# Kernel optimization log

Measured on AMD Instinct MI355X. Metric: run time of the kernel, lower is better.

## Reference

```python
import jax, jax.numpy as jnp
import numpy as np

N_NODES = 50000
N_EDGES = 800000
HIDDEN = 128
N_TYPES = 4
TIME_STEPS = [2]  # one layer, 2 propagation steps; residuals = {}


def setup_inputs() -> dict:
    key = jax.random.key(0)
    ks = jax.random.split(key, 8)
    std = HIDDEN ** (-0.5)
    states = jax.random.normal(ks[0], (N_NODES, HIDDEN), dtype=jnp.float32)
    etype = jax.random.randint(ks[1], (N_EDGES,), 0, N_TYPES, dtype=jnp.int32)
    src = jax.random.randint(ks[2], (N_EDGES,), 0, N_NODES, dtype=jnp.int32)
    tgt = jax.random.randint(ks[3], (N_EDGES,), 0, N_NODES, dtype=jnp.int32)
    edges = jnp.stack([etype, src, tgt], axis=1)  # [E, 3]: (type, source, target)
    type_weights = std * jax.random.normal(ks[4], (N_TYPES, HIDDEN, HIDDEN), dtype=jnp.float32)
    type_biases = std * jax.random.normal(ks[5], (N_TYPES, HIDDEN), dtype=jnp.float32)
    # Keras GRUCell (reset_after=True): kernel [H,3H], recurrent_kernel [H,3H], bias [2,3H]
    gru_kernel = std * jax.random.normal(ks[6], (HIDDEN, 3 * HIDDEN), dtype=jnp.float32)
    k7, k8 = jax.random.split(ks[7])
    gru_rec_kernel = std * jax.random.normal(k7, (HIDDEN, 3 * HIDDEN), dtype=jnp.float32)
    gru_bias = std * jax.random.normal(k8, (2, 3 * HIDDEN), dtype=jnp.float32)
    return {"states": states, "edges": edges, "type_weights": type_weights,
            "type_biases": type_biases, "gru_kernel": gru_kernel,
            "gru_rec_kernel": gru_rec_kernel, "gru_bias": gru_bias}


def _gru_cell(x, h, kernel, rec_kernel, bias):
    # Keras GRUCell with reset_after=True, tanh / sigmoid activations
    mx = x @ kernel + bias[0]          # [N, 3H]
    mh = h @ rec_kernel + bias[1]      # [N, 3H]
    xz, xr, xh = jnp.split(mx, 3, axis=-1)
    rz, rr, rh = jnp.split(mh, 3, axis=-1)
    z = jax.nn.sigmoid(xz + rz)
    r = jax.nn.sigmoid(xr + rr)
    hh = jnp.tanh(xh + r * rh)
    return z * h + (1.0 - z) * hh


def _propagate(h, etype, src, tgt, type_weights, type_biases, kernel, rec_kernel, bias):
    n_nodes = h.shape[0]
    xs = h[src]  # [E, H] gather of source states
    msg_e = jnp.zeros_like(xs)
    for t in range(N_TYPES):  # small fixed loop over edge types
        mask = (etype == t).astype(h.dtype)[:, None]
        msg_e = msg_e + mask * (xs @ type_weights[t] + type_biases[t])
    messages = jax.ops.segment_sum(msg_e, tgt, num_segments=n_nodes)  # scatter-add
    return _gru_cell(messages, h, kernel, rec_kernel, bias)


def reference(states, edges, type_weights, type_biases, gru_kernel, gru_rec_kernel, gru_bias):
    etype, src, tgt = edges[:, 0], edges[:, 1], edges[:, 2]
    h = states
    for steps in TIME_STEPS:  # single layer here (residuals empty)
        for _ in range(steps):
            h = _propagate(h, etype, src, tgt, type_weights, type_biases,
                           gru_kernel, gru_rec_kernel, gru_bias)
    return h
```

## Files before the change

kernel.cpp:

```cpp
#include <hip/hip_runtime.h>
#include <stdint.h>

namespace {
constexpr int kNodes = 50000;
constexpr int kEdges = 800000;
constexpr int kHid   = 128;
constexpr int kCap   = 64;
constexpr int kBlocks32 = (kNodes + 31) / 32;
constexpr int kFillBlocks = kEdges / 256;
constexpr int kTfBlocks = kBlocks32;

constexpr size_t oCounts = 0;
constexpr size_t oBpack  = 200704;
constexpr size_t oEll    = 856064;
constexpr size_t oMsg    = 13656064;
constexpr size_t oY      = 26456064;
constexpr size_t kWsNeeded   = oY + 51200000;
constexpr size_t kWsFallback = oY;

constexpr size_t bKhi = 0,      bKlo = 98304,  bRhi = 196608,
                 bRlo = 294912, bWhi = 393216, bWlo = 524288;
}

typedef __attribute__((ext_vector_type(8))) short short8;
typedef __attribute__((ext_vector_type(4))) float f32x4;

union ABFrag { short8 v; uint16_t u[8]; uint4 q; };

__device__ __forceinline__ uint16_t f2bf(float x) {
  uint32_t u = __float_as_uint(x);
  return (uint16_t)((u + 0x7FFFu + ((u >> 16) & 1u)) >> 16);
}
__device__ __forceinline__ float bf2f(uint16_t h) {
  return __uint_as_float(((uint32_t)h) << 16);
}

__device__ __forceinline__ float fast_rcp(float x) {
#if __has_builtin(__builtin_amdgcn_rcpf)
  return __builtin_amdgcn_rcpf(x);
#else
  return 1.f / x;
#endif
}
__device__ __forceinline__ float fast_exp2(float x) {
#if __has_builtin(__builtin_amdgcn_exp2f)
  return __builtin_amdgcn_exp2f(x);
#else
  return exp2f(x);
#endif
}
__device__ __forceinline__ float sigf(float x) {
  return fast_rcp(1.f + fast_exp2(-1.4426950408889634f * x));
}
__device__ __forceinline__ float tanh_fast(float x) {
  x = fminf(fmaxf(x, -10.f), 10.f);
  const float t = fast_exp2(2.8853900817779268f * x);
  return (t - 1.f) * fast_rcp(t + 1.f);
}

__device__ __forceinline__ int swz_pi(int p) {
  return (p & 64) | ((p & 3) << 4) | ((p >> 2) & 15);
}

__global__ __launch_bounds__(256) void pack_b_kernel(
    const float* __restrict__ K,
    const float* __restrict__ R,
    const float* __restrict__ W,
    uint16_t* __restrict__ bp) {
  const int idx = blockIdx.x * 256 + threadIdx.x;
  uint16_t* khi = bp + bKhi / 2;
  uint16_t* klo = bp + bKlo / 2;
  uint16_t* rhi = bp + bRhi / 2;
  uint16_t* rlo = bp + bRlo / 2;
  uint16_t* whi = bp + bWhi / 2;
  uint16_t* wlo = bp + bWlo / 2;
  if (idx < 128 * 384) {
    const int k = idx / 384, c = idx % 384;
    const int ksrc = swz_pi(k);
    const int kt = k >> 5, quad = (k >> 3) & 3, j = k & 7;
    const int nt = c >> 4, ln = (c & 15) | (quad << 4);
    const size_t o = ((size_t)(kt * 24 + nt) * 64 + ln) * 8 + j;
    const float kv = K[ksrc * 384 + c];
    const float rv = R[k * 384 + c];
    const uint16_t kh = f2bf(kv), rh = f2bf(rv);
    khi[o] = kh; klo[o] = f2bf(kv - bf2f(kh));
    rhi[o] = rh; rlo[o] = f2bf(rv - bf2f(rh));
  } else if (idx < 128 * 384 + 128 * 512) {
    const int i2 = idx - 128 * 384;
    const int k = i2 / 512, c = i2 % 512;
    const int t = c >> 7, cc = c & 127;
    const float wv = W[((size_t)t * 128 + k) * 128 + cc];
    const int kt = k >> 5, quad = (k >> 3) & 3, j = k & 7;
    const int nt = c >> 4, ln = (c & 15) | (quad << 4);
    const size_t o = ((size_t)(kt * 32 + nt) * 64 + ln) * 8 + j;
    const uint16_t wh = f2bf(wv);
    whi[o] = wh; wlo[o] = f2bf(wv - bf2f(wh));
  }
}

__device__ __forceinline__ void fill_ell_body(const int* __restrict__ edges,
                                              int* __restrict__ cnt,
                                              unsigned* __restrict__ ell,
                                              int e) {
  if (e < kEdges) {
    const int et  = edges[e * 3 + 0];
    const int src = edges[e * 3 + 1];
    const int tgt = edges[e * 3 + 2];
    const int pos = atomicAdd(&cnt[tgt], 1);
    if (pos < kCap) ell[(size_t)tgt * kCap + pos] = (unsigned)(src * 4 + et);
  }
}

__global__ __launch_bounds__(256) void fill_ell_kernel(
    const int* __restrict__ edges, int* __restrict__ cnt,
    unsigned* __restrict__ ell) {
  fill_ell_body(edges, cnt, ell, blockIdx.x * 256 + threadIdx.x);
}

__device__ __forceinline__ void transform_wave(
    const float* __restrict__ h, const uint16_t* __restrict__ bp,
    const float* __restrict__ TB, uint16_t* __restrict__ y16,
    int node0, int w, int lane) {
  const int col16 = lane & 15, quad = lane >> 4;
  const uint4* __restrict__ Whi = (const uint4*)(bp + bWhi / 2);
  const uint4* __restrict__ Wlo = (const uint4*)(bp + bWlo / 2);

  bool mok[2];
#pragma unroll
  for (int m = 0; m < 2; ++m) mok[m] = (node0 + m * 16) < kNodes;

  f32x4 acc[8][2];
#pragma unroll
  for (int nt = 0; nt < 8; ++nt)
#pragma unroll
    for (int m = 0; m < 2; ++m) acc[nt][m] = (f32x4){0.f, 0.f, 0.f, 0.f};

  const float* hrow = h + (size_t)(node0 + col16) * kHid + quad * 8;

#pragma unroll
  for (int kt = 0; kt < 4; ++kt) {
    float4 araw[2][2];
#pragma unroll
    for (int m = 0; m < 2; ++m) {
      if (mok[m]) {
        araw[m][0] = *(const float4*)(hrow + (size_t)m * 16 * kHid + kt * 32);
        araw[m][1] = *(const float4*)(hrow + (size_t)m * 16 * kHid + kt * 32 + 4);
      } else {
        araw[m][0] = make_float4(0.f, 0.f, 0.f, 0.f);
        araw[m][1] = araw[m][0];
      }
    }
    ABFrag bh[8], bl[8];
#pragma unroll
    for (int nt = 0; nt < 8; ++nt) {
      bh[nt].q = Whi[(size_t)(kt * 32 + w * 8 + nt) * 64 + lane];
      bl[nt].q = Wlo[(size_t)(kt * 32 + w * 8 + nt) * 64 + lane];
    }
    ABFrag ah[2], al[2];
#pragma unroll
    for (int m = 0; m < 2; ++m) {
      const float vv[8] = {araw[m][0].x, araw[m][0].y, araw[m][0].z, araw[m][0].w,
                           araw[m][1].x, araw[m][1].y, araw[m][1].z, araw[m][1].w};
#pragma unroll
      for (int j = 0; j < 8; ++j) {
        const uint16_t t = f2bf(vv[j]);
        ah[m].u[j] = t; al[m].u[j] = f2bf(vv[j] - bf2f(t));
      }
    }
#pragma unroll
    for (int nt = 0; nt < 8; ++nt) {
#pragma unroll
      for (int m = 0; m < 2; ++m) {
        f32x4 c = acc[nt][m];
        c = __builtin_amdgcn_mfma_f32_16x16x32_bf16(ah[m].v, bh[nt].v, c, 0, 0, 0);
        c = __builtin_amdgcn_mfma_f32_16x16x32_bf16(ah[m].v, bl[nt].v, c, 0, 0, 0);
        c = __builtin_amdgcn_mfma_f32_16x16x32_bf16(al[m].v, bh[nt].v, c, 0, 0, 0);
        acc[nt][m] = c;
      }
    }
  }

#pragma unroll
  for (int g = 0; g < 2; ++g) {
    float bias[4];
#pragma unroll
    for (int s = 0; s < 4; ++s) bias[s] = TB[w * 128 + (g * 4 + s) * 16 + col16];
#pragma unroll
    for (int m = 0; m < 2; ++m) {
      if (!mok[m]) continue;
#pragma unroll
      for (int r = 0; r < 4; ++r) {
        const int node = node0 + m * 16 + quad * 4 + r;
        const uint32_t lo = (uint32_t)f2bf(acc[g * 4 + 0][m][r] + bias[0]) |
                            ((uint32_t)f2bf(acc[g * 4 + 1][m][r] + bias[1]) << 16);
        const uint32_t hi = (uint32_t)f2bf(acc[g * 4 + 2][m][r] + bias[2]) |
                            ((uint32_t)f2bf(acc[g * 4 + 3][m][r] + bias[3]) << 16);
        *(uint2*)&y16[(size_t)node * 512 + w * 128 + g * 64 + col16 * 4] =
            make_uint2(lo, hi);
      }
    }
  }
}

__global__ __launch_bounds__(64, 2) void transform_mfma(
    const float* __restrict__ h, const uint16_t* __restrict__ bp,
    const float* __restrict__ TB, uint16_t* __restrict__ y16) {
  transform_wave(h, bp, TB, y16, (blockIdx.x >> 2) * 32, blockIdx.x & 3,
                 threadIdx.x);
}

__global__ __launch_bounds__(256, 2) void tf1_fill_kernel(
    const float* __restrict__ h, const uint16_t* __restrict__ bp,
    const float* __restrict__ TB, uint16_t* __restrict__ y16,
    const int* __restrict__ edges, int* __restrict__ cnt,
    unsigned* __restrict__ ell) {
  if (blockIdx.x < kTfBlocks) {
    transform_wave(h, bp, TB, y16, blockIdx.x * 32, threadIdx.x >> 6,
                   threadIdx.x & 63);
  } else {
    fill_ell_body(edges, cnt, ell,
                  (blockIdx.x - kTfBlocks) * 256 + threadIdx.x);
  }
}

__global__ __launch_bounds__(256) void gather_kernel(
    const uint32_t* __restrict__ y2,
    const uint32_t* __restrict__ ell,
    const int* __restrict__ counts,
    uint32_t* __restrict__ msg2) {
  const int tid = threadIdx.x;
  const int lane = tid & 63;
  const int v = blockIdx.x * 4 + (tid >> 6);
  const int cnt = min(counts[v], kCap);
  const uint32_t* __restrict__ row = ell + (size_t)v * kCap;
  float a0 = 0.f, a1 = 0.f;
  int e = 0;
  for (; e + 8 <= cnt; e += 8) {
    uint32_t p[8], u[8];
#pragma unroll
    for (int i = 0; i < 8; ++i) p[i] = row[e + i];
#pragma unroll
    for (int i = 0; i < 8; ++i) u[i] = y2[(size_t)p[i] * 64 + lane];
#pragma unroll
    for (int i = 0; i < 8; ++i) {
      a0 += __uint_as_float(u[i] << 16);
      a1 += __uint_as_float(u[i] & 0xFFFF0000u);
    }
  }
  for (; e < cnt; ++e) {
    const uint32_t p = row[e];
    const uint32_t u = y2[(size_t)p * 64 + lane];
    a0 += __uint_as_float(u << 16);
    a1 += __uint_as_float(u & 0xFFFF0000u);
  }
  msg2[(size_t)v * 64 + lane] = (uint32_t)f2bf(a0) | ((uint32_t)f2bf(a1) << 16);
}

__global__ __launch_bounds__(256, 2) void gru_mfma(
    const uint16_t* __restrict__ msg16,
    const float* __restrict__ hin,
    const uint16_t* __restrict__ bp,
    const float* __restrict__ gb,
    float* __restrict__ hout) {
  const int tid = threadIdx.x;
  const int w = tid >> 6;
  const int lane = tid & 63;
  const int col16 = lane & 15, quad = lane >> 4;
  const int node0 = blockIdx.x * 32;

  const uint4* __restrict__ Khi = (const uint4*)(bp + bKhi / 2);
  const uint4* __restrict__ Klo = (const uint4*)(bp + bKlo / 2);
  const uint4* __restrict__ Rhi = (const uint4*)(bp + bRhi / 2);
  const uint4* __restrict__ Rlo = (const uint4*)(bp + bRlo / 2);

  bool mok[2];
#pragma unroll
  for (int m = 0; m < 2; ++m) mok[m] = (node0 + m * 16) < kNodes;

  f32x4 aZ[2][2], aR[2][2], aX[2][2], aH[2][2];
#pragma unroll
  for (int i = 0; i < 2; ++i)
#pragma unroll
    for (int m = 0; m < 2; ++m) {
      aZ[i][m] = (f32x4){0.f, 0.f, 0.f, 0.f};
      aR[i][m] = aZ[i][m]; aX[i][m] = aZ[i][m]; aH[i][m] = aZ[i][m];
    }

  const uint16_t* mrow = msg16 + (size_t)(node0 + col16) * kHid + quad * 8;
  const float* hrow = hin + (size_t)(node0 + col16) * kHid + quad * 8;

#pragma unroll
  for (int kt = 0; kt < 4; ++kt) {
    uint4 mraw[2]; float4 hraw[2][2];
#pragma unroll
    for (int m = 0; m < 2; ++m) {
      if (mok[m]) {
        mraw[m] = *(const uint4*)(mrow + (size_t)m * 16 * kHid + kt * 32);
        hraw[m][0] = *(const float4*)(hrow + (size_t)m * 16 * kHid + kt * 32);
        hraw[m][1] = *(const float4*)(hrow + (size_t)m * 16 * kHid + kt * 32 + 4);
      } else {
        mraw[m] = make_uint4(0, 0, 0, 0);
        hraw[m][0] = make_float4(0.f, 0.f, 0.f, 0.f);
        hraw[m][1] = hraw[m][0];
      }
    }
    ABFrag BZ[2][4], BR[2][4], BH[2][4];
#pragma unroll
    for (int lnt = 0; lnt < 2; ++lnt) {
      const int ntc = w * 2 + lnt;
      const size_t oz = (size_t)(kt * 24 + ntc) * 64 + lane;
      const size_t orr = (size_t)(kt * 24 + 8 + ntc) * 64 + lane;
      const size_t oh = (size_t)(kt * 24 + 16 + ntc) * 64 + lane;
      BZ[lnt][0].q = Khi[oz];  BZ[lnt][1].q = Klo[oz];
      BZ[lnt][2].q = Rhi[oz];  BZ[lnt][3].q = Rlo[oz];
      BR[lnt][0].q = Khi[orr]; BR[lnt][1].q = Klo[orr];
      BR[lnt][2].q = Rhi[orr]; BR[lnt][3].q = Rlo[orr];
      BH[lnt][0].q = Khi[oh];  BH[lnt][1].q = Klo[oh];
      BH[lnt][2].q = Rhi[oh];  BH[lnt][3].q = Rlo[oh];
    }
    ABFrag mh[2], hh[2];
#pragma unroll
    for (int m = 0; m < 2; ++m) {
      mh[m].q = mraw[m];
      const float vv[8] = {hraw[m][0].x, hraw[m][0].y, hraw[m][0].z, hraw[m][0].w,
                           hraw[m][1].x, hraw[m][1].y, hraw[m][1].z, hraw[m][1].w};
#pragma unroll
      for (int j = 0; j < 8; ++j) hh[m].u[j] = f2bf(vv[j]);
    }
#pragma unroll
    for (int lnt = 0; lnt < 2; ++lnt) {
#pragma unroll
      for (int m = 0; m < 2; ++m) {
        f32x4 z = aZ[lnt][m];
        z = __builtin_amdgcn_mfma_f32_16x16x32_bf16(mh[m].v, BZ[lnt][0].v, z, 0, 0, 0);
        z = __builtin_amdgcn_mfma_f32_16x16x32_bf16(mh[m].v, BZ[lnt][1].v, z, 0, 0, 0);
        z = __builtin_amdgcn_mfma_f32_16x16x32_bf16(hh[m].v, BZ[lnt][2].v, z, 0, 0, 0);
        z = __builtin_amdgcn_mfma_f32_16x16x32_bf16(hh[m].v, BZ[lnt][3].v, z, 0, 0, 0);
        aZ[lnt][m] = z;
        f32x4 r = aR[lnt][m];
        r = __builtin_amdgcn_mfma_f32_16x16x32_bf16(mh[m].v, BR[lnt][0].v, r, 0, 0, 0);
        r = __builtin_amdgcn_mfma_f32_16x16x32_bf16(mh[m].v, BR[lnt][1].v, r, 0, 0, 0);
        r = __builtin_amdgcn_mfma_f32_16x16x32_bf16(hh[m].v, BR[lnt][2].v, r, 0, 0, 0);
        r = __builtin_amdgcn_mfma_f32_16x16x32_bf16(hh[m].v, BR[lnt][3].v, r, 0, 0, 0);
        aR[lnt][m] = r;
        f32x4 x = aX[lnt][m];
        x = __builtin_amdgcn_mfma_f32_16x16x32_bf16(mh[m].v, BH[lnt][0].v, x, 0, 0, 0);
        x = __builtin_amdgcn_mfma_f32_16x16x32_bf16(mh[m].v, BH[lnt][1].v, x, 0, 0, 0);
        aX[lnt][m] = x;
        f32x4 y = aH[lnt][m];
        y = __builtin_amdgcn_mfma_f32_16x16x32_bf16(hh[m].v, BH[lnt][2].v, y, 0, 0, 0);
        y = __builtin_amdgcn_mfma_f32_16x16x32_bf16(hh[m].v, BH[lnt][3].v, y, 0, 0, 0);
        aH[lnt][m] = y;
      }
    }
  }

  __syncthreads();

#pragma unroll
  for (int lnt = 0; lnt < 2; ++lnt) {
    const int c = (w * 2 + lnt) * 16 + col16;
    const float bz = gb[c] + gb[384 + c];
    const float br = gb[128 + c] + gb[512 + c];
    const float bx = gb[256 + c];
    const float bh = gb[640 + c];
#pragma unroll
    for (int m = 0; m < 2; ++m) {
      if (!mok[m]) continue;
#pragma unroll
      for (int r = 0; r < 4; ++r) {
        const int node = node0 + m * 16 + quad * 4 + r;
        const float hp = hin[(size_t)node * kHid + c];
        const float z = sigf(aZ[lnt][m][r] + bz);
        const float rr = sigf(aR[lnt][m][r] + br);
        const float hh = tanh_fast(aX[lnt][m][r] + bx + rr * (aH[lnt][m][r] + bh));
        hout[(size_t)node * kHid + c] = z * hp + (1.f - z) * hh;
      }
    }
  }
}


__global__ __launch_bounds__(256, 2) void message_fb_kernel(
    const float* __restrict__ hin,
    const unsigned* __restrict__ ell,
    const int* __restrict__ counts,
    const float* __restrict__ W,
    const float* __restrict__ TB,
    float* __restrict__ msg) {
  __shared__ float S[32 * 512];
  __shared__ int D[32][4];
  const int tid = threadIdx.x;
  {
    const int g = tid >> 7;
    const int j = tid & 127;
    for (int i = 0; i < 16; ++i) {
      const int nl = g * 16 + i;
      const int v = blockIdx.x * 32 + nl;
      if (v >= kNodes) break;
      const int cnt = min(counts[v], kCap);
      const unsigned* __restrict__ row = ell + (size_t)v * kCap;
      float a0 = 0.f, a1 = 0.f, a2 = 0.f, a3 = 0.f;
      int d0 = 0, d1 = 0, d2 = 0, d3 = 0;
      for (int e = 0; e < cnt; ++e) {
        const unsigned p = row[e];
        const int src = (int)(p >> 2);
        const int t = (int)(p & 3u);
        const float val = hin[(size_t)src * kHid + j];
        a0 += (t == 0) ? val : 0.f;
        a1 += (t == 1) ? val : 0.f;
        a2 += (t == 2) ? val : 0.f;
        a3 += (t == 3) ? val : 0.f;
        d0 += (t == 0); d1 += (t == 1); d2 += (t == 2); d3 += (t == 3);
      }
      float* Sn = &S[nl * 512];
      Sn[j] = a0; Sn[128 + j] = a1; Sn[256 + j] = a2; Sn[384 + j] = a3;
      if (j == 0) { D[nl][0] = d0; D[nl][1] = d1; D[nl][2] = d2; D[nl][3] = d3; }
    }
  }
  __syncthreads();

  const int lane = tid & 31;
  const int jj = lane * 4;
  const int n0 = (tid >> 5) * 4;
  float acc[4][4] = {};
  const float4* __restrict__ W4 = (const float4*)W;
  for (int tk = 0; tk < 512; tk += 4) {
    const float4 w0 = W4[(size_t)(tk + 0) * 32 + lane];
    const float4 w1 = W4[(size_t)(tk + 1) * 32 + lane];
    const float4 w2 = W4[(size_t)(tk + 2) * 32 + lane];
    const float4 w3 = W4[(size_t)(tk + 3) * 32 + lane];
#pragma unroll
    for (int n = 0; n < 4; ++n) {
      const float4 s = *(const float4*)&S[(n0 + n) * 512 + tk];
      acc[n][0] += s.x * w0.x + s.y * w1.x + s.z * w2.x + s.w * w3.x;
      acc[n][1] += s.x * w0.y + s.y * w1.y + s.z * w2.y + s.w * w3.y;
      acc[n][2] += s.x * w0.z + s.y * w1.z + s.z * w2.z + s.w * w3.z;
      acc[n][3] += s.x * w0.w + s.y * w1.w + s.z * w2.w + s.w * w3.w;
    }
  }
  const float4 B0 = *(const float4*)&TB[0 * 128 + jj];
  const float4 B1 = *(const float4*)&TB[1 * 128 + jj];
  const float4 B2 = *(const float4*)&TB[2 * 128 + jj];
  const float4 B3 = *(const float4*)&TB[3 * 128 + jj];
#pragma unroll
  for (int n = 0; n < 4; ++n) {
    const int v = blockIdx.x * 32 + n0 + n;
    if (v < kNodes) {
      float4 o;
      const float d0 = (float)D[n0 + n][0], d1 = (float)D[n0 + n][1];
      const float d2 = (float)D[n0 + n][2], d3 = (float)D[n0 + n][3];
      o.x = acc[n][0] + d0 * B0.x + d1 * B1.x + d2 * B2.x + d3 * B3.x;
      o.y = acc[n][1] + d0 * B0.y + d1 * B1.y + d2 * B2.y + d3 * B3.y;
      o.z = acc[n][2] + d0 * B0.z + d1 * B1.z + d2 * B2.z + d3 * B3.z;
      o.w = acc[n][3] + d0 * B0.w + d1 * B1.w + d2 * B2.w + d3 * B3.w;
      *(float4*)&msg[(size_t)v * kHid + jj] = o;
    }
  }
}

__global__ __launch_bounds__(256, 2) void gru_fb_kernel(
    const float* __restrict__ msg,
    const float* __restrict__ hin,
    const float* __restrict__ K,
    const float* __restrict__ R,
    const float* __restrict__ gb,
    float* __restrict__ hout) {
  __shared__ float At[2][16][68];
  __shared__ float Bt[2][16][384];
  const int tid = threadIdx.x;
  const int node0 = blockIdx.x * 64;
  const int cg = tid >> 4;
  const int ng = tid & 15;

  float accZ[4][8] = {}, accR[4][8] = {}, accXH[4][8] = {}, accRH[4][8] = {};
  const float4* __restrict__ K4 = (const float4*)K;
  const float4* __restrict__ R4 = (const float4*)R;
  const int sn = tid >> 2;
  const int sj = tid & 3;

  for (int k0 = 0; k0 < 128; k0 += 16) {
    __syncthreads();
    {
      float4 vm = make_float4(0.f, 0.f, 0.f, 0.f);
      float4 vh = vm;
      const int node = node0 + sn;
      if (node < kNodes) {
        vm = *(const float4*)&msg[(size_t)node * kHid + k0 + sj * 4];
        vh = *(const float4*)&hin[(size_t)node * kHid + k0 + sj * 4];
      }
      At[0][sj * 4 + 0][sn] = vm.x; At[0][sj * 4 + 1][sn] = vm.y;
      At[0][sj * 4 + 2][sn] = vm.z; At[0][sj * 4 + 3][sn] = vm.w;
      At[1][sj * 4 + 0][sn] = vh.x; At[1][sj * 4 + 1][sn] = vh.y;
      At[1][sj * 4 + 2][sn] = vh.z; At[1][sj * 4 + 3][sn] = vh.w;
    }
#pragma unroll
    for (int i = 0; i < 6; ++i) {
      const int idx = tid + i * 256;
      const int row = idx / 96;
      const int c4 = idx - row * 96;
      *(float4*)&Bt[0][row][c4 * 4] = K4[(size_t)(k0 + row) * 96 + c4];
      *(float4*)&Bt[1][row][c4 * 4] = R4[(size_t)(k0 + row) * 96 + c4];
    }
    __syncthreads();

    for (int kk = 0; kk < 16; ++kk) {
      const float4 am4 = *(const float4*)&At[0][kk][ng * 4];
      const float4 ah4 = *(const float4*)&At[1][kk][ng * 4];
      const float am[4] = {am4.x, am4.y, am4.z, am4.w};
      const float ah[4] = {ah4.x, ah4.y, ah4.z, ah4.w};
      const int cb = cg * 8;
#pragma unroll
      for (int gset = 0; gset < 3; ++gset) {
        const int off = gset * 128 + cb;
        const float4 k0v = *(const float4*)&Bt[0][kk][off];
        const float4 k1v = *(const float4*)&Bt[0][kk][off + 4];
        const float4 r0v = *(const float4*)&Bt[1][kk][off];
        const float4 r1v = *(const float4*)&Bt[1][kk][off + 4];
        const float bk[8] = {k0v.x, k0v.y, k0v.z, k0v.w, k1v.x, k1v.y, k1v.z, k1v.w};
        const float br[8] = {r0v.x, r0v.y, r0v.z, r0v.w, r1v.x, r1v.y, r1v.z, r1v.w};
        if (gset == 0) {
#pragma unroll
          for (int n = 0; n < 4; ++n)
#pragma unroll
            for (int c = 0; c < 8; ++c) accZ[n][c] += am[n] * bk[c] + ah[n] * br[c];
        } else if (gset == 1) {
#pragma unroll
          for (int n = 0; n < 4; ++n)
#pragma unroll
            for (int c = 0; c < 8; ++c) accR[n][c] += am[n] * bk[c] + ah[n] * br[c];
        } else {
#pragma unroll
          for (int n = 0; n < 4; ++n)
#pragma unroll
            for (int c = 0; c < 8; ++c) {
              accXH[n][c] += am[n] * bk[c];
              accRH[n][c] += ah[n] * br[c];
            }
        }
      }
    }
  }

  const int cb = cg * 8;
#pragma unroll
  for (int n = 0; n < 4; ++n) {
    const int node = node0 + ng * 4 + n;
    if (node >= kNodes) continue;
    float o[8];
#pragma unroll
    for (int c = 0; c < 8; ++c) {
      const float z = sigf(accZ[n][c] + gb[cb + c] + gb[384 + cb + c]);
      const float r = sigf(accR[n][c] + gb[128 + cb + c] + gb[512 + cb + c]);
      const float hh = tanh_fast(accXH[n][c] + gb[256 + cb + c] +
                                 r * (accRH[n][c] + gb[640 + cb + c]));
      const float hp = hin[(size_t)node * kHid + cb + c];
      o[c] = z * hp + (1.f - z) * hh;
    }
    *(float4*)&hout[(size_t)node * kHid + cb]     = make_float4(o[0], o[1], o[2], o[3]);
    *(float4*)&hout[(size_t)node * kHid + cb + 4] = make_float4(o[4], o[5], o[6], o[7]);
  }
}

extern "C" void kernel_launch(void* const* d_in, const int* in_sizes, int n_in,
                              void* d_out, int out_size, void* d_ws, size_t ws_size,
                              hipStream_t stream) {
  const float* states = (const float*)d_in[0];
  const int*   edges  = (const int*)d_in[1];
  const float* W      = (const float*)d_in[2];
  const float* TB     = (const float*)d_in[3];
  const float* K      = (const float*)d_in[4];
  const float* R      = (const float*)d_in[5];
  const float* gb     = (const float*)d_in[6];
  float* out = (float*)d_out;

  if (ws_size < kWsFallback) return;

  char* ws = (char*)d_ws;
  int*      counts  = (int*)(ws + oCounts);
  uint16_t* bpack   = (uint16_t*)(ws + oBpack);
  unsigned* ell     = (unsigned*)(ws + oEll);
  float*    msgf    = (float*)(ws + oMsg);
  uint16_t* msg16   = (uint16_t*)(ws + oMsg);
  uint32_t* msg2    = (uint32_t*)(ws + oMsg);
  uint16_t* y16     = (uint16_t*)(ws + oY);
  uint32_t* y2      = (uint32_t*)(ws + oY);

  hipMemsetAsync(counts, 0, 200704, stream);

  if (ws_size >= kWsNeeded) {
    pack_b_kernel<<<448, 256, 0, stream>>>(K, R, W, bpack);
    const int ga_blocks = kNodes / 4;
    const int tf_blocks = kBlocks32 * 4;
    tf1_fill_kernel<<<kTfBlocks + kFillBlocks, 256, 0, stream>>>(
        states, bpack, TB, y16, edges, counts, ell);
    gather_kernel<<<ga_blocks, 256, 0, stream>>>(y2, (uint32_t*)ell, counts, msg2);
    gru_mfma<<<kBlocks32, 256, 0, stream>>>(msg16, states, bpack, gb, out);
    transform_mfma<<<tf_blocks, 64, 0, stream>>>(out, bpack, TB, y16);
    gather_kernel<<<ga_blocks, 256, 0, stream>>>(y2, (uint32_t*)ell, counts, msg2);
    gru_mfma<<<kBlocks32, 256, 0, stream>>>(msg16, out, bpack, gb, out);
  } else {
    if (ws_size < oMsg + (size_t)kNodes * kHid * 4) return;
    fill_ell_kernel<<<kFillBlocks, 256, 0, stream>>>(edges, counts, ell);
    const int msg_blocks = (kNodes + 31) / 32;
    const int gru_blocks = (kNodes + 63) / 64;
    message_fb_kernel<<<msg_blocks, 256, 0, stream>>>(states, ell, counts, W, TB,
                                                      msgf);
    gru_fb_kernel<<<gru_blocks, 256, 0, stream>>>(msgf, states, K, R, gb, out);
    message_fb_kernel<<<msg_blocks, 256, 0, stream>>>(out, ell, counts, W, TB,
                                                      msgf);
    gru_fb_kernel<<<gru_blocks, 256, 0, stream>>>(msgf, out, K, R, gb, out);
  }
}
```

Measured before the change: 358.3 us.

## Fuse aggregate-then-transform message pass with GRU into one kernel per step

Replaces the transform-then-gather pipeline (per-type 512-wide bf16 Y buffer, gather, separate GRU) with a single fused kernel per step. Each block sums raw fp32 source states per edge type into LDS and counts degrees per type. It then runs the type-weight matmul on the aggregated [32x512] tile with split-bf16 MFMA, adds degree-weighted biases, and feeds the result straight into the GRU MFMA from LDS. This removes the large Y write/read and the msg round trip and cuts kernel launches. The cost is gathering fp32 rows (512 B per edge instead of 256 B bf16), a larger K=512 matmul per node, and big LDS use that may lower occupancy.

New measurement: 690.2 us. 92.7% more time.

```diff
diff --git a/kernel.cpp b/kernel.cpp
--- a/kernel.cpp
+++ b/kernel.cpp
@@ -8,15 +8,13 @@
 constexpr int kCap   = 64;
 constexpr int kBlocks32 = (kNodes + 31) / 32;
 constexpr int kFillBlocks = kEdges / 256;
-constexpr int kTfBlocks = kBlocks32;
+constexpr int kPackBlocks = 448;
 
 constexpr size_t oCounts = 0;
 constexpr size_t oBpack  = 200704;
 constexpr size_t oEll    = 856064;
-constexpr size_t oMsg    = 13656064;
-constexpr size_t oY      = 26456064;
-constexpr size_t kWsNeeded   = oY + 51200000;
-constexpr size_t kWsFallback = oY;
+constexpr size_t oH1     = 13656064;
+constexpr size_t kWsNeeded = oH1 + 25600000;
 
 constexpr size_t bKhi = 0,      bKlo = 98304,  bRhi = 196608,
                  bRlo = 294912, bWhi = 393216, bWlo = 524288;
@@ -62,12 +60,41 @@
   return (p & 64) | ((p & 3) << 4) | ((p >> 2) & 15);
 }
 
-__global__ __launch_bounds__(256) void pack_b_kernel(
-    const float* __restrict__ K,
-    const float* __restrict__ R,
-    const float* __restrict__ W,
-    uint16_t* __restrict__ bp) {
-  const int idx = blockIdx.x * 256 + threadIdx.x;
+__device__ __forceinline__ void split8(const float* p, ABFrag& hi, ABFrag& lo) {
+  const float4 a0 = *(const float4*)p;
+  const float4 a1 = *(const float4*)(p + 4);
+  const float v[8] = {a0.x, a0.y, a0.z, a0.w, a1.x, a1.y, a1.z, a1.w};
+#pragma unroll
+  for (int j = 0; j < 8; ++j) {
+    const uint16_t t = f2bf(v[j]);
+    hi.u[j] = t; lo.u[j] = f2bf(v[j] - bf2f(t));
+  }
+}
+__device__ __forceinline__ void conv8(const float* p, ABFrag& hi) {
+  const float4 a0 = *(const float4*)p;
+  const float4 a1 = *(const float4*)(p + 4);
+  const float v[8] = {a0.x, a0.y, a0.z, a0.w, a1.x, a1.y, a1.z, a1.w};
+#pragma unroll
+  for (int j = 0; j < 8; ++j) hi.u[j] = f2bf(v[j]);
+}
+
+__global__ __launch_bounds__(256) void pack_fill_kernel(
+    const int* __restrict__ edges, int* __restrict__ cnt,
+    unsigned* __restrict__ ell,
+    const float* __restrict__ K, const float* __restrict__ R,
+    const float* __restrict__ W, uint16_t* __restrict__ bp) {
+  if (blockIdx.x < kFillBlocks) {
+    const int e = blockIdx.x * 256 + threadIdx.x;
+    if (e < kEdges) {
+      const int et  = edges[e * 3 + 0];
+      const int src = edges[e * 3 + 1];
+      const int tgt = edges[e * 3 + 2];
+      const int pos = atomicAdd(&cnt[tgt], 1);
+      if (pos < kCap) ell[(size_t)tgt * kCap + pos] = (unsigned)(src * 4 + et);
+    }
+    return;
+  }
+  const int idx = (blockIdx.x - kFillBlocks) * 256 + threadIdx.x;
   uint16_t* khi = bp + bKhi / 2;
   uint16_t* klo = bp + bKlo / 2;
   uint16_t* rhi = bp + bRhi / 2;
@@ -87,187 +114,134 @@
     rhi[o] = rh; rlo[o] = f2bf(rv - bf2f(rh));
   } else if (idx < 128 * 384 + 128 * 512) {
     const int i2 = idx - 128 * 384;
-    const int k = i2 / 512, c = i2 % 512;
-    const int t = c >> 7, cc = c & 127;
-    const float wv = W[((size_t)t * 128 + k) * 128 + cc];
-    const int kt = k >> 5, quad = (k >> 3) & 3, j = k & 7;
+    const int kk = i2 >> 7;
+    const int c  = i2 & 127;
+    const int t = kk >> 7, k = kk & 127;
+    const float wv = W[((size_t)t * 128 + k) * 128 + c];
+    const int kt2 = kk >> 5, quad = (kk >> 3) & 3, j = kk & 7;
     const int nt = c >> 4, ln = (c & 15) | (quad << 4);
-    const size_t o = ((size_t)(kt * 32 + nt) * 64 + ln) * 8 + j;
+    const size_t o = ((size_t)(kt2 * 8 + nt) * 64 + ln) * 8 + j;
     const uint16_t wh = f2bf(wv);
     whi[o] = wh; wlo[o] = f2bf(wv - bf2f(wh));
   }
 }
 
-__device__ __forceinline__ void fill_ell_body(const int* __restrict__ edges,
-                                              int* __restrict__ cnt,
-                                              unsigned* __restrict__ ell,
-                                              int e) {
-  if (e < kEdges) {
-    const int et  = edges[e * 3 + 0];
-    const int src = edges[e * 3 + 1];
-    const int tgt = edges[e * 3 + 2];
-    const int pos = atomicAdd(&cnt[tgt], 1);
-    if (pos < kCap) ell[(size_t)tgt * kCap + pos] = (unsigned)(src * 4 + et);
-  }
-}
-
-__global__ __launch_bounds__(256) void fill_ell_kernel(
-    const int* __restrict__ edges, int* __restrict__ cnt,
-    unsigned* __restrict__ ell) {
-  fill_ell_body(edges, cnt, ell, blockIdx.x * 256 + threadIdx.x);
-}
-
-__device__ __forceinline__ void transform_wave(
-    const float* __restrict__ h, const uint16_t* __restrict__ bp,
-    const float* __restrict__ TB, uint16_t* __restrict__ y16,
-    int node0, int w, int lane) {
+__global__ __launch_bounds__(256, 2) void fused_msg_gru(
+    const float* __restrict__ hin,
+    const unsigned* __restrict__ ell,
+    const int* __restrict__ counts,
+    const uint16_t* __restrict__ bp,
+    const float* __restrict__ TB,
+    const float* __restrict__ gb,
+    float* __restrict__ hout) {
+  __shared__ __align__(16) float S[32 * 516];
+  __shared__ int D[32][4];
+  const int tid = threadIdx.x;
+  const int node0 = blockIdx.x * 32;
+
+  {
+    const int g = tid >> 7;
+    const int j = tid & 127;
+    for (int i = 0; i < 16; ++i) {
+      const int nl = g * 16 + i;
+      const int v = node0 + nl;
+      float a0 = 0.f, a1 = 0.f, a2 = 0.f, a3 = 0.f;
+      int d0 = 0, d1 = 0, d2 = 0, d3 = 0;
+      if (v < kNodes) {
+        const int cnt = min(counts[v], kCap);
+        const unsigned* __restrict__ row = ell + (size_t)v * kCap;
+        int e = 0;
+        for (; e + 8 <= cnt; e += 8) {
+          unsigned p[8]; float val[8];
+#pragma unroll
+          for (int q = 0; q < 8; ++q) p[q] = row[e + q];
+#pragma unroll
+          for (int q = 0; q < 8; ++q)
+            val[q] = hin[(size_t)(p[q] >> 2) * kHid + j];
+#pragma unroll
+          for (int q = 0; q < 8; ++q) {
+            const int t = (int)(p[q] & 3u);
+            a0 += (t == 0) ? val[q] : 0.f; a1 += (t == 1) ? val[q] : 0.f;
+            a2 += (t == 2) ? val[q] : 0.f; a3 += (t == 3) ? val[q] : 0.f;
+            d0 += (t == 0); d1 += (t == 1); d2 += (t == 2); d3 += (t == 3);
+          }
+        }
+        for (; e < cnt; ++e) {
+          const unsigned p = row[e];
+          const float val = hin[(size_t)(p >> 2) * kHid + j];
+          const int t = (int)(p & 3u);
+          a0 += (t == 0) ? val : 0.f; a1 += (t == 1) ? val : 0.f;
+          a2 += (t == 2) ? val : 0.f; a3 += (t == 3) ? val : 0.f;
+          d0 += (t == 0); d1 += (t == 1); d2 += (t == 2); d3 += (t == 3);
+        }
+      }
+      float* Sn = &S[nl * 516];
+      Sn[j] = a0; Sn[128 + j] = a1; Sn[256 + j] = a2; Sn[384 + j] = a3;
+      if (j == 0) { D[nl][0] = d0; D[nl][1] = d1; D[nl][2] = d2; D[nl][3] = d3; }
+    }
+  }
+  __syncthreads();
+
+  const int w = tid >> 6;
+  const int lane = tid & 63;
   const int col16 = lane & 15, quad = lane >> 4;
   const uint4* __restrict__ Whi = (const uint4*)(bp + bWhi / 2);
   const uint4* __restrict__ Wlo = (const uint4*)(bp + bWlo / 2);
 
-  bool mok[2];
-#pragma unroll
-  for (int m = 0; m < 2; ++m) mok[m] = (node0 + m * 16) < kNodes;
-
-  f32x4 acc[8][2];
-#pragma unroll
-  for (int nt = 0; nt < 8; ++nt)
-#pragma unroll
-    for (int m = 0; m < 2; ++m) acc[nt][m] = (f32x4){0.f, 0.f, 0.f, 0.f};
-
-  const float* hrow = h + (size_t)(node0 + col16) * kHid + quad * 8;
-
-#pragma unroll
-  for (int kt = 0; kt < 4; ++kt) {
-    float4 araw[2][2];
-#pragma unroll
-    for (int m = 0; m < 2; ++m) {
-      if (mok[m]) {
-        araw[m][0] = *(const float4*)(hrow + (size_t)m * 16 * kHid + kt * 32);
-        araw[m][1] = *(const float4*)(hrow + (size_t)m * 16 * kHid + kt * 32 + 4);
-      } else {
-        araw[m][0] = make_float4(0.f, 0.f, 0.f, 0.f);
-        araw[m][1] = araw[m][0];
-      }
-    }
-    ABFrag bh[8], bl[8];
-#pragma unroll
-    for (int nt = 0; nt < 8; ++nt) {
-      bh[nt].q = Whi[(size_t)(kt * 32 + w * 8 + nt) * 64 + lane];
-      bl[nt].q = Wlo[(size_t)(kt * 32 + w * 8 + nt) * 64 + lane];
-    }
+  f32x4 acc[2][2];
+#pragma unroll
+  for (int i = 0; i < 2; ++i)
+#pragma unroll
+    for (int m = 0; m < 2; ++m) acc[i][m] = (f32x4){0.f, 0.f, 0.f, 0.f};
+
+  for (int kt2 = 0; kt2 < 16; ++kt2) {
     ABFrag ah[2], al[2];
 #pragma unroll
-    for (int m = 0; m < 2; ++m) {
-      const float vv[8] = {araw[m][0].x, araw[m][0].y, araw[m][0].z, araw[m][0].w,
-                           araw[m][1].x, araw[m][1].y, araw[m][1].z, araw[m][1].w};
-#pragma unroll
-      for (int j = 0; j < 8; ++j) {
-        const uint16_t t = f2bf(vv[j]);
-        ah[m].u[j] = t; al[m].u[j] = f2bf(vv[j] - bf2f(t));
-      }
-    }
-#pragma unroll
-    for (int nt = 0; nt < 8; ++nt) {
+    for (int m = 0; m < 2; ++m)
+      split8(&S[(size_t)(col16 + m * 16) * 516 + kt2 * 32 + quad * 8],
+             ah[m], al[m]);
+    ABFrag bh[2], bl[2];
+#pragma unroll
+    for (int lnt = 0; lnt < 2; ++lnt) {
+      const size_t o = (size_t)(kt2 * 8 + w * 2 + lnt) * 64 + lane;
+      bh[lnt].q = Whi[o]; bl[lnt].q = Wlo[o];
+    }
+#pragma unroll
+    for (int lnt = 0; lnt < 2; ++lnt)
 #pragma unroll
       for (int m = 0; m < 2; ++m) {
-        f32x4 c = acc[nt][m];
-        c = __builtin_amdgcn_mfma_f32_16x16x32_bf16(ah[m].v, bh[nt].v, c, 0, 0, 0);
-        c = __builtin_amdgcn_mfma_f32_16x16x32_bf16(ah[m].v, bl[nt].v, c, 0, 0, 0);
-        c = __builtin_amdgcn_mfma_f32_16x16x32_bf16(al[m].v, bh[nt].v, c, 0, 0, 0);
-        acc[nt][m] = c;
-      }
-    }
-  }
-
-#pragma unroll
-  for (int g = 0; g < 2; ++g) {
-    float bias[4];
-#pragma unroll
-    for (int s = 0; s < 4; ++s) bias[s] = TB[w * 128 + (g * 4 + s) * 16 + col16];
-#pragma unroll
-    for (int m = 0; m < 2; ++m) {
-      if (!mok[m]) continue;
+        f32x4 c = acc[lnt][m];
+        c = __builtin_amdgcn_mfma_f32_16x16x32_bf16(ah[m].v, bh[lnt].v, c, 0, 0, 0);
+        c = __builtin_amdgcn_mfma_f32_16x16x32_bf16(ah[m].v, bl[lnt].v, c, 0, 0, 0);
+        c = __builtin_amdgcn_mfma_f32_16x16x32_bf16(al[m].v, bh[lnt].v, c, 0, 0, 0);
+        acc[lnt][m] = c;
+      }
+  }
+  __syncthreads();
+
+  uint16_t* msgT16 = (uint16_t*)S;
+#pragma unroll
+  for (int lnt = 0; lnt < 2; ++lnt) {
+    const int c = (w * 2 + lnt) * 16 + col16;
+    const float tb0 = TB[c], tb1 = TB[128 + c], tb2 = TB[256 + c],
+                tb3 = TB[384 + c];
+    const int p = ((c >> 6) << 6) | (col16 << 2) | ((c >> 4) & 3);
+    const int kt = p >> 5, hi3 = (p >> 3) & 3, jq = p & 7;
+#pragma unroll
+    for (int m = 0; m < 2; ++m)
 #pragma unroll
       for (int r = 0; r < 4; ++r) {
-        const int node = node0 + m * 16 + quad * 4 + r;
-        const uint32_t lo = (uint32_t)f2bf(acc[g * 4 + 0][m][r] + bias[0]) |
-                            ((uint32_t)f2bf(acc[g * 4 + 1][m][r] + bias[1]) << 16);
-        const uint32_t hi = (uint32_t)f2bf(acc[g * 4 + 2][m][r] + bias[2]) |
-                            ((uint32_t)f2bf(acc[g * 4 + 3][m][r] + bias[3]) << 16);
-        *(uint2*)&y16[(size_t)node * 512 + w * 128 + g * 64 + col16 * 4] =
-            make_uint2(lo, hi);
-      }
-    }
-  }
-}
-
-__global__ __launch_bounds__(64, 2) void transform_mfma(
-    const float* __restrict__ h, const uint16_t* __restrict__ bp,
-    const float* __restrict__ TB, uint16_t* __restrict__ y16) {
-  transform_wave(h, bp, TB, y16, (blockIdx.x >> 2) * 32, blockIdx.x & 3,
-                 threadIdx.x);
-}
-
-__global__ __launch_bounds__(256, 2) void tf1_fill_kernel(
-    const float* __restrict__ h, const uint16_t* __restrict__ bp,
-    const float* __restrict__ TB, uint16_t* __restrict__ y16,
-    const int* __restrict__ edges, int* __restrict__ cnt,
-    unsigned* __restrict__ ell) {
-  if (blockIdx.x < kTfBlocks) {
-    transform_wave(h, bp, TB, y16, blockIdx.x * 32, threadIdx.x >> 6,
-                   threadIdx.x & 63);
-  } else {
-    fill_ell_body(edges, cnt, ell,
-                  (blockIdx.x - kTfBlocks) * 256 + threadIdx.x);
-  }
-}
-
-__global__ __launch_bounds__(256) void gather_kernel(
-    const uint32_t* __restrict__ y2,
-    const uint32_t* __restrict__ ell,
-    const int* __restrict__ counts,
-    uint32_t* __restrict__ msg2) {
-  const int tid = threadIdx.x;
-  const int lane = tid & 63;
-  const int v = blockIdx.x * 4 + (tid >> 6);
-  const int cnt = min(counts[v], kCap);
-  const uint32_t* __restrict__ row = ell + (size_t)v * kCap;
-  float a0 = 0.f, a1 = 0.f;
-  int e = 0;
-  for (; e + 8 <= cnt; e += 8) {
-    uint32_t p[8], u[8];
-#pragma unroll
-    for (int i = 0; i < 8; ++i) p[i] = row[e + i];
-#pragma unroll
-    for (int i = 0; i < 8; ++i) u[i] = y2[(size_t)p[i] * 64 + lane];
-#pragma unroll
-    for (int i = 0; i < 8; ++i) {
-      a0 += __uint_as_float(u[i] << 16);
-      a1 += __uint_as_float(u[i] & 0xFFFF0000u);
-    }
-  }
-  for (; e < cnt; ++e) {
-    const uint32_t p = row[e];
-    const uint32_t u = y2[(size_t)p * 64 + lane];
-    a0 += __uint_as_float(u << 16);
-    a1 += __uint_as_float(u & 0xFFFF0000u);
-  }
-  msg2[(size_t)v * 64 + lane] = (uint32_t)f2bf(a0) | ((uint32_t)f2bf(a1) << 16);
-}
-
-__global__ __launch_bounds__(256, 2) void gru_mfma(
-    const uint16_t* __restrict__ msg16,
-    const float* __restrict__ hin,
-    const uint16_t* __restrict__ bp,
-    const float* __restrict__ gb,
-    float* __restrict__ hout) {
-  const int tid = threadIdx.x;
-  const int w = tid >> 6;
-  const int lane = tid & 63;
-  const int col16 = lane & 15, quad = lane >> 4;
-  const int node0 = blockIdx.x * 32;
-
+        const int n16 = quad * 4 + r;
+        const int nl = m * 16 + n16;
+        const float bias = (float)D[nl][0] * tb0 + (float)D[nl][1] * tb1 +
+                           (float)D[nl][2] * tb2 + (float)D[nl][3] * tb3;
+        msgT16[((m * 4 + kt) * 64 + hi3 * 16 + n16) * 8 + jq] =
+            f2bf(acc[lnt][m][r] + bias);
+      }
+  }
+  __syncthreads();
+
+  const uint4* __restrict__ msgQ = (const uint4*)msgT16;
   const uint4* __restrict__ Khi = (const uint4*)(bp + bKhi / 2);
   const uint4* __restrict__ Klo = (const uint4*)(bp + bKlo / 2);
   const uint4* __restrict__ Rhi = (const uint4*)(bp + bRhi / 2);
@@ -286,20 +260,17 @@
       aR[i][m] = aZ[i][m]; aX[i][m] = aZ[i][m]; aH[i][m] = aZ[i][m];
     }
 
-  const uint16_t* mrow = msg16 + (size_t)(node0 + col16) * kHid + quad * 8;
   const float* hrow = hin + (size_t)(node0 + col16) * kHid + quad * 8;
 
 #pragma unroll
   for (int kt = 0; kt < 4; ++kt) {
-    uint4 mraw[2]; float4 hraw[2][2];
+    float4 hraw[2][2];
 #pragma unroll
     for (int m = 0; m < 2; ++m) {
       if (mok[m]) {
-        mraw[m] = *(const uint4*)(mrow + (size_t)m * 16 * kHid + kt * 32);
         hraw[m][0] = *(const float4*)(hrow + (size_t)m * 16 * kHid + kt * 32);
         hraw[m][1] = *(const float4*)(hrow + (size_t)m * 16 * kHid + kt * 32 + 4);
       } else {
-        mraw[m] = make_uint4(0, 0, 0, 0);
         hraw[m][0] = make_float4(0.f, 0.f, 0.f, 0.f);
         hraw[m][1] = hraw[m][0];
       }
@@ -321,7 +292,7 @@
     ABFrag mh[2], hh[2];
 #pragma unroll
     for (int m = 0; m < 2; ++m) {
-      mh[m].q = mraw[m];
+      mh[m].q = msgQ[(m * 4 + kt) * 64 + lane];
       const float vv[8] = {hraw[m][0].x, hraw[m][0].y, hraw[m][0].z, hraw[m][0].w,
                            hraw[m][1].x, hraw[m][1].y, hraw[m][1].z, hraw[m][1].w};
 #pragma unroll
@@ -355,8 +326,6 @@
     }
   }
 
-  __syncthreads();
-
 #pragma unroll
   for (int lnt = 0; lnt < 2; ++lnt) {
     const int c = (w * 2 + lnt) * 16 + col16;
@@ -377,188 +346,6 @@
         hout[(size_t)node * kHid + c] = z * hp + (1.f - z) * hh;
       }
     }
-  }
-}
-
-
-__global__ __launch_bounds__(256, 2) void message_fb_kernel(
-    const float* __restrict__ hin,
-    const unsigned* __restrict__ ell,
-    const int* __restrict__ counts,
-    const float* __restrict__ W,
-    const float* __restrict__ TB,
-    float* __restrict__ msg) {
-  __shared__ float S[32 * 512];
-  __shared__ int D[32][4];
-  const int tid = threadIdx.x;
-  {
-    const int g = tid >> 7;
-    const int j = tid & 127;
-    for (int i = 0; i < 16; ++i) {
-      const int nl = g * 16 + i;
-      const int v = blockIdx.x * 32 + nl;
-      if (v >= kNodes) break;
-      const int cnt = min(counts[v], kCap);
-      const unsigned* __restrict__ row = ell + (size_t)v * kCap;
-      float a0 = 0.f, a1 = 0.f, a2 = 0.f, a3 = 0.f;
-      int d0 = 0, d1 = 0, d2 = 0, d3 = 0;
-      for (int e = 0; e < cnt; ++e) {
-        const unsigned p = row[e];
-        const int src = (int)(p >> 2);
-        const int t = (int)(p & 3u);
-        const float val = hin[(size_t)src * kHid + j];
-        a0 += (t == 0) ? val : 0.f;
-        a1 += (t == 1) ? val : 0.f;
-        a2 += (t == 2) ? val : 0.f;
-        a3 += (t == 3) ? val : 0.f;
-        d0 += (t == 0); d1 += (t == 1); d2 += (t == 2); d3 += (t == 3);
-      }
-      float* Sn = &S[nl * 512];
-      Sn[j] = a0; Sn[128 + j] = a1; Sn[256 + j] = a2; Sn[384 + j] = a3;
-      if (j == 0) { D[nl][0] = d0; D[nl][1] = d1; D[nl][2] = d2; D[nl][3] = d3; }
-    }
-  }
-  __syncthreads();
-
-  const int lane = tid & 31;
-  const int jj = lane * 4;
-  const int n0 = (tid >> 5) * 4;
-  float acc[4][4] = {};
-  const float4* __restrict__ W4 = (const float4*)W;
-  for (int tk = 0; tk < 512; tk += 4) {
-    const float4 w0 = W4[(size_t)(tk + 0) * 32 + lane];
-    const float4 w1 = W4[(size_t)(tk + 1) * 32 + lane];
-    const float4 w2 = W4[(size_t)(tk + 2) * 32 + lane];
-    const float4 w3 = W4[(size_t)(tk + 3) * 32 + lane];
-#pragma unroll
-    for (int n = 0; n < 4; ++n) {
-      const float4 s = *(const float4*)&S[(n0 + n) * 512 + tk];
-      acc[n][0] += s.x * w0.x + s.y * w1.x + s.z * w2.x + s.w * w3.x;
-      acc[n][1] += s.x * w0.y + s.y * w1.y + s.z * w2.y + s.w * w3.y;
-      acc[n][2] += s.x * w0.z + s.y * w1.z + s.z * w2.z + s.w * w3.z;
-      acc[n][3] += s.x * w0.w + s.y * w1.w + s.z * w2.w + s.w * w3.w;
-    }
-  }
-  const float4 B0 = *(const float4*)&TB[0 * 128 + jj];
-  const float4 B1 = *(const float4*)&TB[1 * 128 + jj];
-  const float4 B2 = *(const float4*)&TB[2 * 128 + jj];
-  const float4 B3 = *(const float4*)&TB[3 * 128 + jj];
-#pragma unroll
-  for (int n = 0; n < 4; ++n) {
-    const int v = blockIdx.x * 32 + n0 + n;
-    if (v < kNodes) {
-      float4 o;
-      const float d0 = (float)D[n0 + n][0], d1 = (float)D[n0 + n][1];
-      const float d2 = (float)D[n0 + n][2], d3 = (float)D[n0 + n][3];
-      o.x = acc[n][0] + d0 * B0.x + d1 * B1.x + d2 * B2.x + d3 * B3.x;
-      o.y = acc[n][1] + d0 * B0.y + d1 * B1.y + d2 * B2.y + d3 * B3.y;
-      o.z = acc[n][2] + d0 * B0.z + d1 * B1.z + d2 * B2.z + d3 * B3.z;
-      o.w = acc[n][3] + d0 * B0.w + d1 * B1.w + d2 * B2.w + d3 * B3.w;
-      *(float4*)&msg[(size_t)v * kHid + jj] = o;
-    }
-  }
-}
-
-__global__ __launch_bounds__(256, 2) void gru_fb_kernel(
-    const float* __restrict__ msg,
-    const float* __restrict__ hin,
-    const float* __restrict__ K,
-    const float* __restrict__ R,
-    const float* __restrict__ gb,
-    float* __restrict__ hout) {
-  __shared__ float At[2][16][68];
-  __shared__ float Bt[2][16][384];
-  const int tid = threadIdx.x;
-  const int node0 = blockIdx.x * 64;
-  const int cg = tid >> 4;
-  const int ng = tid & 15;
-
-  float accZ[4][8] = {}, accR[4][8] = {}, accXH[4][8] = {}, accRH[4][8] = {};
-  const float4* __restrict__ K4 = (const float4*)K;
-  const float4* __restrict__ R4 = (const float4*)R;
-  const int sn = tid >> 2;
-  const int sj = tid & 3;
-
-  for (int k0 = 0; k0 < 128; k0 += 16) {
-    __syncthreads();
-    {
-      float4 vm = make_float4(0.f, 0.f, 0.f, 0.f);
-      float4 vh = vm;
-      const int node = node0 + sn;
-      if (node < kNodes) {
-        vm = *(const float4*)&msg[(size_t)node * kHid + k0 + sj * 4];
-        vh = *(const float4*)&hin[(size_t)node * kHid + k0 + sj * 4];
-      }
-      At[0][sj * 4 + 0][sn] = vm.x; At[0][sj * 4 + 1][sn] = vm.y;
-      At[0][sj * 4 + 2][sn] = vm.z; At[0][sj * 4 + 3][sn] = vm.w;
-      At[1][sj * 4 + 0][sn] = vh.x; At[1][sj * 4 + 1][sn] = vh.y;
-      At[1][sj * 4 + 2][sn] = vh.z; At[1][sj * 4 + 3][sn] = vh.w;
-    }
-#pragma unroll
-    for (int i = 0; i < 6; ++i) {
-      const int idx = tid + i * 256;
-      const int row = idx / 96;
-      const int c4 = idx - row * 96;
-      *(float4*)&Bt[0][row][c4 * 4] = K4[(size_t)(k0 + row) * 96 + c4];
-      *(float4*)&Bt[1][row][c4 * 4] = R4[(size_t)(k0 + row) * 96 + c4];
-    }
-    __syncthreads();
-
-    for (int kk = 0; kk < 16; ++kk) {
-      const float4 am4 = *(const float4*)&At[0][kk][ng * 4];
-      const float4 ah4 = *(const float4*)&At[1][kk][ng * 4];
-      const float am[4] = {am4.x, am4.y, am4.z, am4.w};
-      const float ah[4] = {ah4.x, ah4.y, ah4.z, ah4.w};
-      const int cb = cg * 8;
-#pragma unroll
-      for (int gset = 0; gset < 3; ++gset) {
-        const int off = gset * 128 + cb;
-        const float4 k0v = *(const float4*)&Bt[0][kk][off];
-        const float4 k1v = *(const float4*)&Bt[0][kk][off + 4];
-        const float4 r0v = *(const float4*)&Bt[1][kk][off];
-        const float4 r1v = *(const float4*)&Bt[1][kk][off + 4];
-        const float bk[8] = {k0v.x, k0v.y, k0v.z, k0v.w, k1v.x, k1v.y, k1v.z, k1v.w};
-        const float br[8] = {r0v.x, r0v.y, r0v.z, r0v.w, r1v.x, r1v.y, r1v.z, r1v.w};
-        if (gset == 0) {
-#pragma unroll
-          for (int n = 0; n < 4; ++n)
-#pragma unroll
-            for (int c = 0; c < 8; ++c) accZ[n][c] += am[n] * bk[c] + ah[n] * br[c];
-        } else if (gset == 1) {
-#pragma unroll
-          for (int n = 0; n < 4; ++n)
-#pragma unroll
-            for (int c = 0; c < 8; ++c) accR[n][c] += am[n] * bk[c] + ah[n] * br[c];
-        } else {
-#pragma unroll
-          for (int n = 0; n < 4; ++n)
-#pragma unroll
-            for (int c = 0; c < 8; ++c) {
-              accXH[n][c] += am[n] * bk[c];
-              accRH[n][c] += ah[n] * br[c];
-            }
-        }
-      }
-    }
-  }
-
-  const int cb = cg * 8;
-#pragma unroll
-  for (int n = 0; n < 4; ++n) {
-    const int node = node0 + ng * 4 + n;
-    if (node >= kNodes) continue;
-    float o[8];
-#pragma unroll
-    for (int c = 0; c < 8; ++c) {
-      const float z = sigf(accZ[n][c] + gb[cb + c] + gb[384 + cb + c]);
-      const float r = sigf(accR[n][c] + gb[128 + cb + c] + gb[512 + cb + c]);
-      const float hh = tanh_fast(accXH[n][c] + gb[256 + cb + c] +
-                                 r * (accRH[n][c] + gb[640 + cb + c]));
-      const float hp = hin[(size_t)node * kHid + cb + c];
-      o[c] = z * hp + (1.f - z) * hh;
-    }
-    *(float4*)&hout[(size_t)node * kHid + cb]     = make_float4(o[0], o[1], o[2], o[3]);
-    *(float4*)&hout[(size_t)node * kHid + cb + 4] = make_float4(o[4], o[5], o[6], o[7]);
   }
 }
 
@@ -574,41 +361,19 @@
   const float* gb     = (const float*)d_in[6];
   float* out = (float*)d_out;
 
-  if (ws_size < kWsFallback) return;
+  if (ws_size < kWsNeeded) return;
 
   char* ws = (char*)d_ws;
-  int*      counts  = (int*)(ws + oCounts);
-  uint16_t* bpack   = (uint16_t*)(ws + oBpack);
-  unsigned* ell     = (unsigned*)(ws + oEll);
-  float*    msgf    = (float*)(ws + oMsg);
-  uint16_t* msg16   = (uint16_t*)(ws + oMsg);
-  uint32_t* msg2    = (uint32_t*)(ws + oMsg);
-  uint16_t* y16     = (uint16_t*)(ws + oY);
-  uint32_t* y2      = (uint32_t*)(ws + oY);
+  int*      counts = (int*)(ws + oCounts);
+  uint16_t* bpack  = (uint16_t*)(ws + oBpack);
+  unsigned* ell    = (unsigned*)(ws + oEll);
+  float*    h1     = (float*)(ws + oH1);
 
   hipMemsetAsync(counts, 0, 200704, stream);
-
-  if (ws_size >= kWsNeeded) {
-    pack_b_kernel<<<448, 256, 0, stream>>>(K, R, W, bpack);
-    const int ga_blocks = kNodes / 4;
-    const int tf_blocks = kBlocks32 * 4;
-    tf1_fill_kernel<<<kTfBlocks + kFillBlocks, 256, 0, stream>>>(
-        states, bpack, TB, y16, edges, counts, ell);
-    gather_kernel<<<ga_blocks, 256, 0, stream>>>(y2, (uint32_t*)ell, counts, msg2);
-    gru_mfma<<<kBlocks32, 256, 0, stream>>>(msg16, states, bpack, gb, out);
-    transform_mfma<<<tf_blocks, 64, 0, stream>>>(out, bpack, TB, y16);
-    gather_kernel<<<ga_blocks, 256, 0, stream>>>(y2, (uint32_t*)ell, counts, msg2);
-    gru_mfma<<<kBlocks32, 256, 0, stream>>>(msg16, out, bpack, gb, out);
-  } else {
-    if (ws_size < oMsg + (size_t)kNodes * kHid * 4) return;
-    fill_ell_kernel<<<kFillBlocks, 256, 0, stream>>>(edges, counts, ell);
-    const int msg_blocks = (kNodes + 31) / 32;
-    const int gru_blocks = (kNodes + 63) / 64;
-    message_fb_kernel<<<msg_blocks, 256, 0, stream>>>(states, ell, counts, W, TB,
-                                                      msgf);
-    gru_fb_kernel<<<gru_blocks, 256, 0, stream>>>(msgf, states, K, R, gb, out);
-    message_fb_kernel<<<msg_blocks, 256, 0, stream>>>(out, ell, counts, W, TB,
-                                                      msgf);
-    gru_fb_kernel<<<gru_blocks, 256, 0, stream>>>(msgf, out, K, R, gb, out);
-  }
-}
+  pack_fill_kernel<<<kFillBlocks + kPackBlocks, 256, 0, stream>>>(
+      edges, counts, ell, K, R, W, bpack);
+  fused_msg_gru<<<kBlocks32, 256, 0, stream>>>(states, ell, counts, bpack,
+                                               TB, gb, h1);
+  fused_msg_gru<<<kBlocks32, 256, 0, stream>>>(h1, ell, counts, bpack,
+                                               TB, gb, out);
+}
```
